# Kernel tuning notes

Hardware: AMD Instinct MI355X
Metric: run time of the kernel (lower is better)

Reference implementation:

```python
import jax, jax.numpy as jnp
from jax import lax
import numpy as np


def _gru_layer(X, mask, W, U, b):
    """Keras GRU (reset_after=True, gate order [z|r|h]) with Keras-style masking.

    X: [B,T,F] float, mask: [B,T] bool, W: [F,3u], U: [u,3u], b: [2,3u].
    At masked steps the state (== output for GRU) is carried over unchanged.
    Returns (outputs [B,T,u], final_state [B,u]).
    """
    B, T, _ = X.shape
    u = U.shape[0]
    # Precompute input projections for all timesteps (cuDNN-style).
    Xp = jnp.einsum('btf,fg->btg', X, W) + b[0]  # [B,T,3u]

    def step(h, inp):
        x_t, m_t = inp  # x_t: [B,3u], m_t: [B]
        rec = h @ U + b[1]  # [B,3u]
        xz, xr, xh = jnp.split(x_t, 3, axis=-1)
        rz, rr, rh = jnp.split(rec, 3, axis=-1)
        z = jax.nn.sigmoid(xz + rz)
        r = jax.nn.sigmoid(xr + rr)
        hh = jnp.tanh(xh + r * rh)
        h_new = z * h + (1.0 - z) * hh
        h_new = jnp.where(m_t[:, None], h_new, h)  # carry state at masked steps
        return h_new, h_new

    h0 = jnp.zeros((B, u), X.dtype)
    h_final, outs = lax.scan(step, h0, (jnp.swapaxes(Xp, 0, 1), mask.T))
    return jnp.swapaxes(outs, 0, 1), h_final


def setup_inputs() -> dict:
    key = jax.random.key(0)
    ks = jax.random.split(key, 12)
    B, T, F = 64, 1024, 16
    H, E = 256, 256
    vals = jax.random.randint(ks[0], (B, T, F), 0, 20, dtype=jnp.int32)
    # variable-length sequences padded with -1
    lengths = jax.random.randint(ks[1], (B,), T // 4, T + 1)
    valid = jnp.arange(T)[None, :] < lengths[:, None]
    batch = jnp.where(valid[:, :, None], vals, jnp.int32(-1))
    SCALE = 0.05

    def w(k, shape):
        return jax.random.normal(k, shape, jnp.float32) * SCALE

    return {
        'batch': batch,
        'W0': w(ks[2], (F, 3 * H)), 'U0': w(ks[3], (H, 3 * H)), 'b0': jnp.zeros((2, 3 * H), jnp.float32),
        'W1': w(ks[4], (H, 3 * H)), 'U1': w(ks[5], (H, 3 * H)), 'b1': jnp.zeros((2, 3 * H), jnp.float32),
        'W2': w(ks[6], (H, 3 * E)), 'U2': w(ks[7], (E, 3 * E)), 'b2': jnp.zeros((2, 3 * E), jnp.float32),
    }


def reference(batch, W0, U0, b0, W1, U1, b1, W2, U2, b2):
    mask = batch[:, :, -1] != -1  # [B,T]
    X = batch.astype(jnp.float32)
    X, _ = _gru_layer(X, mask, W0, U0, b0)
    X, _ = _gru_layer(X, mask, W1, U1, b1)
    out, h = _gru_layer(X, mask, W2, U2, b2)
    return out, h
```

## Files before the change

kernel.cpp:

```cpp
#include <hip/hip_runtime.h>
#include <cstdint>

#define BATCH 64
#define SEQ   1024
#define FEAT  16
#define HID   256
#define GATE  768
#define TC    64
#define LASTC 15
#define NT    512
#define NWRK  64
#define NITEM 192

typedef _Float16 f16x8 __attribute__((ext_vector_type(8)));
typedef float    f32x4 __attribute__((ext_vector_type(4)));

__device__ __forceinline__ float sigmoidf_(float x) { return 1.0f / (1.0f + __expf(-x)); }
__device__ __forceinline__ float tanhf_(float x)    { return 2.0f / (1.0f + __expf(-2.0f * x)) - 1.0f; }

__global__ __launch_bounds__(256) void k_packB(const float* __restrict__ U,
                                               float* __restrict__ Bfrag)
{
    const int tid = blockIdx.x * 256 + threadIdx.x;
    const int ct   = tid >> 9;
    const int kt   = (tid >> 6) & 7;
    const int lane = tid & 63;
    const int g = lane >> 4, i = lane & 15;
    const int col = ct * 16 + i;
    const int k0  = kt * 32 + g * 8;
    union { f16x8 v; float4 f; } u;
#pragma unroll
    for (int e = 0; e < 8; ++e)
        u.v[e] = (_Float16)U[(size_t)(k0 + e) * GATE + col];
    *(float4*)(Bfrag + (size_t)tid * 4) = u.f;
}

struct Params {
    const int*   batch;
    const float *W0, *b0, *b1, *b2;
    const float *Bf0, *Bf1, *Bf2;
    const float *Wp1, *Wp2;
    _Float16 *xp0a, *xp0b, *xp1a, *xp1b, *xp2a, *xp2b;
    _Float16 *y0a, *y0b, *y1a, *y1b;
    float *h0, *h1, *h2;
    float *out, *hfin;
};

__device__ __forceinline__ void gru_body(
    char* smem, const _Float16* __restrict__ xp, const float* __restrict__ Bfrag,
    const float* __restrict__ bb, const int* __restrict__ batch,
    _Float16* __restrict__ yout, float* __restrict__ fout, int obase,
    float* __restrict__ hfinal, float* __restrict__ hstate, int t0, int b)
{
    _Float16 (*hbuf)[HID] = (_Float16 (*)[HID])smem;

    const int T  = threadIdx.x;
    const int w  = T >> 6;
    const int l  = T & 63;
    const int g  = l >> 4;
    const int i  = l & 15;
    const int g1 = g & 1;
    const int c  = 32 * w + i + 16 * g1;

    f16x8 Bf[6][8];
    {
        const int cts[6] = {2 * w, 16 + 2 * w, 32 + 2 * w,
                            2 * w + 1, 17 + 2 * w, 33 + 2 * w};
#pragma unroll
        for (int ci = 0; ci < 6; ++ci)
#pragma unroll
            for (int kt = 0; kt < 8; ++kt) {
                float4 v = *(const float4*)(Bfrag + ((size_t)(cts[ci] * 8 + kt) * 64 + l) * 4);
                Bf[ci][kt] = __builtin_bit_cast(f16x8, v);
            }
    }

    const float bh = bb[GATE + 2 * HID + c];

    float hprev = (t0 == 0) ? 0.0f : hstate[b * HID + c];
    if (l < 32) hbuf[0][32 * w + l] = (_Float16)hprev;

    _Float16 nxz, nxr, nxh; int nmf;
    {
        const _Float16* xrow = xp + ((size_t)b * TC + 0) * GATE;
        nxz = xrow[c]; nxr = xrow[HID + c]; nxh = xrow[2 * HID + c];
        nmf = batch[((size_t)b * SEQ + t0) * FEAT + (FEAT - 1)];
    }
    __syncthreads();

    for (int tl = 0; tl < TC; ++tl) {
        const _Float16 cxz = nxz, cxr = nxr, cxh = nxh;
        const int cmf = nmf;
        {
            const int tn = (tl + 1 < TC) ? tl + 1 : tl;
            const _Float16* xrow = xp + ((size_t)b * TC + tn) * GATE;
            nxz = xrow[c]; nxr = xrow[HID + c]; nxh = xrow[2 * HID + c];
            nmf = batch[((size_t)b * SEQ + t0 + tn) * FEAT + (FEAT - 1)];
        }

        const _Float16* rd = hbuf[tl & 1];

        f32x4 az0 = {0.f, 0.f, 0.f, 0.f}, ar0 = az0, ah0 = az0;
        f32x4 az1 = az0, ar1 = az0, ah1 = az0;
#pragma unroll
        for (int kt = 0; kt < 8; ++kt) {
            const f16x8 a = *(const f16x8*)(rd + kt * 32 + g * 8);
            az0 = __builtin_amdgcn_mfma_f32_16x16x32_f16(a, Bf[0][kt], az0, 0, 0, 0);
            ar0 = __builtin_amdgcn_mfma_f32_16x16x32_f16(a, Bf[1][kt], ar0, 0, 0, 0);
            ah0 = __builtin_amdgcn_mfma_f32_16x16x32_f16(a, Bf[2][kt], ah0, 0, 0, 0);
            az1 = __builtin_amdgcn_mfma_f32_16x16x32_f16(a, Bf[3][kt], az1, 0, 0, 0);
            ar1 = __builtin_amdgcn_mfma_f32_16x16x32_f16(a, Bf[4][kt], ar1, 0, 0, 0);
            ah1 = __builtin_amdgcn_mfma_f32_16x16x32_f16(a, Bf[5][kt], ah1, 0, 0, 0);
        }

        const float az = g1 ? az1[0] : az0[0];
        const float ar = g1 ? ar1[0] : ar0[0];
        const float ah = g1 ? ah1[0] : ah0[0];

        const float z  = sigmoidf_((float)cxz + az);
        const float r  = sigmoidf_((float)cxr + ar);
        const float hh = tanhf_((float)cxh + r * (ah + bh));
        float hn = z * hprev + (1.0f - z) * hh;
        hn = (cmf != -1) ? hn : hprev;
        hprev = hn;

        if (l < 32) {
            if (yout)
                yout[((size_t)b * TC + tl) * HID + 32 * w + l] = (_Float16)hn;
            else
                fout[((size_t)b * SEQ + obase + tl) * HID + 32 * w + l] = hn;
            hbuf[(tl & 1) ^ 1][32 * w + l] = (_Float16)hn;
        }
        asm volatile("s_waitcnt lgkmcnt(0)\n\ts_barrier" ::: "memory");
    }

    if (l < 32) {
        hstate[b * HID + 32 * w + l] = hprev;
        if (hfinal) hfinal[b * HID + 32 * w + l] = hprev;
    }
}

__device__ __forceinline__ void gemm_mfma_body(
    char* smem, const _Float16* __restrict__ Yc, const float* __restrict__ Wp,
    const float* __restrict__ bb, _Float16* __restrict__ xpout, int mt)
{
    _Float16 (*As)[264] = (_Float16 (*)[264])smem;

    const int T = threadIdx.x;
    const int w = T >> 6;
    const int l = T & 63;
    const int g = l >> 4;
    const int i = l & 15;

    {
        const _Float16* src = Yc + (size_t)mt * TC * HID;
#pragma unroll
        for (int q = 0; q < 4; ++q) {
            const int ch  = T * 4 + q;
            const int row = ch >> 5;
            const int ko  = (ch & 31) * 8;
            *(float4*)&As[row][ko] = *(const float4*)(src + (size_t)row * HID + ko);
        }
    }
    __syncthreads();

    f16x8 Af[4][8];
#pragma unroll
    for (int rt = 0; rt < 4; ++rt)
#pragma unroll
        for (int kt = 0; kt < 8; ++kt)
            Af[rt][kt] = *(const f16x8*)&As[rt * 16 + i][kt * 32 + g * 8];

#pragma unroll
    for (int ci = 0; ci < 6; ++ci) {
        const int ct = w * 6 + ci;
        f16x8 Bfr[8];
#pragma unroll
        for (int kt = 0; kt < 8; ++kt) {
            float4 v = *(const float4*)(Wp + ((size_t)(ct * 8 + kt) * 64 + l) * 4);
            Bfr[kt] = __builtin_bit_cast(f16x8, v);
        }
        f32x4 acc[4];
#pragma unroll
        for (int rt = 0; rt < 4; ++rt) acc[rt] = (f32x4){0.f, 0.f, 0.f, 0.f};
#pragma unroll
        for (int kt = 0; kt < 8; ++kt) {
            acc[0] = __builtin_amdgcn_mfma_f32_16x16x32_f16(Af[0][kt], Bfr[kt], acc[0], 0, 0, 0);
            acc[1] = __builtin_amdgcn_mfma_f32_16x16x32_f16(Af[1][kt], Bfr[kt], acc[1], 0, 0, 0);
            acc[2] = __builtin_amdgcn_mfma_f32_16x16x32_f16(Af[2][kt], Bfr[kt], acc[2], 0, 0, 0);
            acc[3] = __builtin_amdgcn_mfma_f32_16x16x32_f16(Af[3][kt], Bfr[kt], acc[3], 0, 0, 0);
        }
        const int n = ct * 16 + i;
        const float bias = bb[n] + ((n < 2 * HID) ? bb[GATE + n] : 0.0f);
#pragma unroll
        for (int rt = 0; rt < 4; ++rt)
#pragma unroll
            for (int r = 0; r < 4; ++r)
                xpout[(size_t)(mt * TC + rt * 16 + 4 * g + r) * GATE + n] =
                    (_Float16)(acc[rt][r] + bias);
    }
    __syncthreads();
}

__device__ __forceinline__ void xp0_body(
    char* smem, const int* __restrict__ batch, const float* __restrict__ W0,
    const float* __restrict__ bb, _Float16* __restrict__ xpout, int t0, int b)
{
    int* bl = (int*)smem;
    const int T = threadIdx.x;
    for (int idx = T; idx < TC * FEAT; idx += NT)
        bl[idx] = batch[((size_t)b * SEQ + t0 + (idx >> 4)) * FEAT + (idx & 15)];
    __syncthreads();

    const int cc0 = T;
    const int cc1 = T + NT;
    const bool two = (cc1 < GATE);

    float w0a[FEAT], w0b[FEAT];
#pragma unroll
    for (int f = 0; f < FEAT; ++f) w0a[f] = W0[f * GATE + cc0];
    if (two) {
#pragma unroll
        for (int f = 0; f < FEAT; ++f) w0b[f] = W0[f * GATE + cc1];
    }
    const float ba = bb[cc0] + ((cc0 < 2 * HID) ? bb[GATE + cc0] : 0.0f);
    const float bc = two ? (bb[cc1] + ((cc1 < 2 * HID) ? bb[GATE + cc1] : 0.0f)) : 0.0f;

    for (int tl = 0; tl < TC; ++tl) {
        float a0 = ba, a1 = bc;
#pragma unroll
        for (int f = 0; f < FEAT; ++f) {
            const float xf = (float)bl[tl * FEAT + f];
            a0 += xf * w0a[f];
            if (two) a1 += xf * w0b[f];
        }
        _Float16* orow = xpout + ((size_t)b * TC + tl) * GATE;
        orow[cc0] = (_Float16)a0;
        if (two) orow[cc1] = (_Float16)a1;
    }
    __syncthreads();
}

__global__ __launch_bounds__(NT, 1) void k_fused(Params P, int d)
{
    __shared__ __align__(16) char smem[64 * 264 * 2];
    const int bid = blockIdx.x;

    if (bid < 64) {
        const int c = d;
        if (c >= 0 && c <= LASTC)
            gru_body(smem, (c & 1) ? P.xp0b : P.xp0a, P.Bf0, P.b0, P.batch,
                     (c & 1) ? P.y0b : P.y0a, nullptr, 0, nullptr, P.h0,
                     c * TC, bid);
    } else if (bid < 128) {
        const int c = d - 2;
        if (c >= 0 && c <= LASTC)
            gru_body(smem, (c & 1) ? P.xp1b : P.xp1a, P.Bf1, P.b1, P.batch,
                     (c & 1) ? P.y1b : P.y1a, nullptr, 0, nullptr, P.h1,
                     c * TC, bid - 64);
    } else if (bid < 192) {
        const int c = d - 4;
        if (c >= 0 && c <= LASTC)
            gru_body(smem, (c & 1) ? P.xp2b : P.xp2a, P.Bf2, P.b2, P.batch,
                     nullptr, P.out, c * TC, (c == LASTC) ? P.hfin : nullptr,
                     P.h2, c * TC, bid - 128);
    } else {
        for (int item = bid - 192; item < NITEM; item += NWRK) {
            if (item < 64) {
                const int c = d + 1;
                if (c >= 0 && c <= LASTC)
                    xp0_body(smem, P.batch, P.W0, P.b0,
                             (c & 1) ? P.xp0b : P.xp0a, c * TC, item);
            } else if (item < 128) {
                const int c = d - 1;
                if (c >= 0 && c <= LASTC)
                    gemm_mfma_body(smem, (c & 1) ? P.y0b : P.y0a, P.Wp1, P.b1,
                                   (c & 1) ? P.xp1b : P.xp1a, item - 64);
            } else {
                const int c = d - 3;
                if (c >= 0 && c <= LASTC)
                    gemm_mfma_body(smem, (c & 1) ? P.y1b : P.y1a, P.Wp2, P.b2,
                                   (c & 1) ? P.xp2b : P.xp2a, item - 128);
            }
        }
    }
}

extern "C" void kernel_launch(void* const* d_in, const int* in_sizes, int n_in,
                              void* d_out, int out_size, void* d_ws, size_t ws_size,
                              hipStream_t stream)
{
    const int*   batch = (const int*)d_in[0];
    const float* W0 = (const float*)d_in[1];
    const float* U0 = (const float*)d_in[2];
    const float* b0 = (const float*)d_in[3];
    const float* W1 = (const float*)d_in[4];
    const float* U1 = (const float*)d_in[5];
    const float* b1 = (const float*)d_in[6];
    const float* W2 = (const float*)d_in[7];
    const float* U2 = (const float*)d_in[8];
    const float* b2 = (const float*)d_in[9];

    float* out  = (float*)d_out;
    float* hfin = out + (size_t)BATCH * SEQ * HID;

    const size_t XPB = (size_t)BATCH * TC * GATE * 2;
    const size_t YB  = (size_t)BATCH * TC * HID * 2;
    const size_t HB  = (size_t)BATCH * HID * 4;
    const size_t BFB = (size_t)48 * 8 * 64 * 4 * 4;

    char* p = (char*)d_ws;
    auto alloc = [&](size_t bytes) { char* q = p; p += (bytes + 255) & ~(size_t)255; return q; };
    _Float16* xp0a = (_Float16*)alloc(XPB);
    _Float16* xp0b = (_Float16*)alloc(XPB);
    _Float16* xp1a = (_Float16*)alloc(XPB);
    _Float16* xp1b = (_Float16*)alloc(XPB);
    _Float16* xp2a = (_Float16*)alloc(XPB);
    _Float16* xp2b = (_Float16*)alloc(XPB);
    _Float16* y0a  = (_Float16*)alloc(YB);
    _Float16* y0b  = (_Float16*)alloc(YB);
    _Float16* y1a  = (_Float16*)alloc(YB);
    _Float16* y1b  = (_Float16*)alloc(YB);
    float* h0  = (float*)alloc(HB);
    float* h1  = (float*)alloc(HB);
    float* h2  = (float*)alloc(HB);
    float* Bf0 = (float*)alloc(BFB);
    float* Bf1 = (float*)alloc(BFB);
    float* Bf2 = (float*)alloc(BFB);
    float* Wp1 = (float*)alloc(BFB);
    float* Wp2 = (float*)alloc(BFB);

    dim3 gpack(48 * 8 * 64 / 256), bpack(256);
    k_packB<<<gpack, bpack, 0, stream>>>(U0, Bf0);
    k_packB<<<gpack, bpack, 0, stream>>>(U1, Bf1);
    k_packB<<<gpack, bpack, 0, stream>>>(U2, Bf2);
    k_packB<<<gpack, bpack, 0, stream>>>(W1, Wp1);
    k_packB<<<gpack, bpack, 0, stream>>>(W2, Wp2);

    Params P;
    P.batch = batch;
    P.W0 = W0; P.b0 = b0; P.b1 = b1; P.b2 = b2;
    P.Bf0 = Bf0; P.Bf1 = Bf1; P.Bf2 = Bf2;
    P.Wp1 = Wp1; P.Wp2 = Wp2;
    P.xp0a = xp0a; P.xp0b = xp0b; P.xp1a = xp1a; P.xp1b = xp1b;
    P.xp2a = xp2a; P.xp2b = xp2b;
    P.y0a = y0a; P.y0b = y0b; P.y1a = y1a; P.y1b = y1b;
    P.h0 = h0; P.h1 = h1; P.h2 = h2;
    P.out = out; P.hfin = hfin;

    for (int d = -1; d <= LASTC + 4; ++d)
        k_fused<<<dim3(256), dim3(NT), 0, stream>>>(P, d);
}
```

Baseline: 1.424 ms.

## Replace per-phase kernel launches with one persistent kernel using grid barriers

The 21 launches of the fused wavefront kernel become a single persistent launch of 256 blocks. Blocks step through the phases themselves and synchronise with an atomic-counter grid barrier. GRU blocks load their recurrent weight fragments into registers once and keep the hidden state in registers between chunks, so the per-launch weight reload and the global h-state round trip go away. The cost is a spin barrier that needs all 256 blocks resident at the same time (one 512-thread block per CU), which risks deadlock if they are not, plus atomic polling overhead at each phase.

```diff
diff --git a/kernel.cpp b/kernel.cpp
--- a/kernel.cpp
+++ b/kernel.cpp
@@ -42,42 +42,31 @@
     const float *Wp1, *Wp2;
     _Float16 *xp0a, *xp0b, *xp1a, *xp1b, *xp2a, *xp2b;
     _Float16 *y0a, *y0b, *y1a, *y1b;
-    float *h0, *h1, *h2;
     float *out, *hfin;
 };
 
-__device__ __forceinline__ void gru_body(
-    char* smem, const _Float16* __restrict__ xp, const float* __restrict__ Bfrag,
-    const float* __restrict__ bb, const int* __restrict__ batch,
+__device__ __forceinline__ void grid_barrier(unsigned* cnt, unsigned target)
+{
+    __threadfence();
+    __syncthreads();
+    if (threadIdx.x == 0) {
+        __hip_atomic_fetch_add(cnt, 1u, __ATOMIC_RELEASE, __HIP_MEMORY_SCOPE_AGENT);
+        while (__hip_atomic_load(cnt, __ATOMIC_ACQUIRE, __HIP_MEMORY_SCOPE_AGENT) < target)
+            __builtin_amdgcn_s_sleep(8);
+    }
+    __syncthreads();
+    __threadfence();
+}
+
+__device__ __forceinline__ void gru_phase(
+    char* smem, const _Float16* __restrict__ xp, const f16x8 (&Bf)[6][8],
+    float bh, const int* __restrict__ batch,
     _Float16* __restrict__ yout, float* __restrict__ fout, int obase,
-    float* __restrict__ hfinal, float* __restrict__ hstate, int t0, int b)
+    float* __restrict__ hfinal, float& hprev, int t0, int b,
+    int w, int l, int g, int g1, int c)
 {
     _Float16 (*hbuf)[HID] = (_Float16 (*)[HID])smem;
 
-    const int T  = threadIdx.x;
-    const int w  = T >> 6;
-    const int l  = T & 63;
-    const int g  = l >> 4;
-    const int i  = l & 15;
-    const int g1 = g & 1;
-    const int c  = 32 * w + i + 16 * g1;
-
-    f16x8 Bf[6][8];
-    {
-        const int cts[6] = {2 * w, 16 + 2 * w, 32 + 2 * w,
-                            2 * w + 1, 17 + 2 * w, 33 + 2 * w};
-#pragma unroll
-        for (int ci = 0; ci < 6; ++ci)
-#pragma unroll
-            for (int kt = 0; kt < 8; ++kt) {
-                float4 v = *(const float4*)(Bfrag + ((size_t)(cts[ci] * 8 + kt) * 64 + l) * 4);
-                Bf[ci][kt] = __builtin_bit_cast(f16x8, v);
-            }
-    }
-
-    const float bh = bb[GATE + 2 * HID + c];
-
-    float hprev = (t0 == 0) ? 0.0f : hstate[b * HID + c];
     if (l < 32) hbuf[0][32 * w + l] = (_Float16)hprev;
 
     _Float16 nxz, nxr, nxh; int nmf;
@@ -134,10 +123,8 @@
         asm volatile("s_waitcnt lgkmcnt(0)\n\ts_barrier" ::: "memory");
     }
 
-    if (l < 32) {
-        hstate[b * HID + 32 * w + l] = hprev;
-        if (hfinal) hfinal[b * HID + 32 * w + l] = hprev;
-    }
+    if (hfinal && l < 32)
+        hfinal[b * HID + 32 * w + l] = hprev;
 }
 
 __device__ __forceinline__ void gemm_mfma_body(
@@ -241,47 +228,82 @@
     __syncthreads();
 }
 
-__global__ __launch_bounds__(NT, 1) void k_fused(Params P, int d)
+__global__ __launch_bounds__(NT, 1) void k_persist(Params P, unsigned* cnt)
 {
     __shared__ __align__(16) char smem[64 * 264 * 2];
     const int bid = blockIdx.x;
-
-    if (bid < 64) {
-        const int c = d;
-        if (c >= 0 && c <= LASTC)
-            gru_body(smem, (c & 1) ? P.xp0b : P.xp0a, P.Bf0, P.b0, P.batch,
-                     (c & 1) ? P.y0b : P.y0a, nullptr, 0, nullptr, P.h0,
-                     c * TC, bid);
-    } else if (bid < 128) {
-        const int c = d - 2;
-        if (c >= 0 && c <= LASTC)
-            gru_body(smem, (c & 1) ? P.xp1b : P.xp1a, P.Bf1, P.b1, P.batch,
-                     (c & 1) ? P.y1b : P.y1a, nullptr, 0, nullptr, P.h1,
-                     c * TC, bid - 64);
-    } else if (bid < 192) {
-        const int c = d - 4;
-        if (c >= 0 && c <= LASTC)
-            gru_body(smem, (c & 1) ? P.xp2b : P.xp2a, P.Bf2, P.b2, P.batch,
-                     nullptr, P.out, c * TC, (c == LASTC) ? P.hfin : nullptr,
-                     P.h2, c * TC, bid - 128);
+    unsigned target = 0;
+
+    if (bid < 192) {
+        const int layer = bid >> 6;
+        const int b     = bid & 63;
+        const float* Bfrag = (layer == 0) ? P.Bf0 : (layer == 1) ? P.Bf1 : P.Bf2;
+        const float* bb    = (layer == 0) ? P.b0  : (layer == 1) ? P.b1  : P.b2;
+
+        const int T  = threadIdx.x;
+        const int w  = T >> 6;
+        const int l  = T & 63;
+        const int g  = l >> 4;
+        const int g1 = g & 1;
+        const int c  = 32 * w + (l & 15) + 16 * g1;
+
+        f16x8 Bf[6][8];
+        {
+            const int cts[6] = {2 * w, 16 + 2 * w, 32 + 2 * w,
+                                2 * w + 1, 17 + 2 * w, 33 + 2 * w};
+#pragma unroll
+            for (int ci = 0; ci < 6; ++ci)
+#pragma unroll
+                for (int kt = 0; kt < 8; ++kt) {
+                    float4 v = *(const float4*)(Bfrag + ((size_t)(cts[ci] * 8 + kt) * 64 + l) * 4);
+                    Bf[ci][kt] = __builtin_bit_cast(f16x8, v);
+                }
+        }
+        const float bh = bb[GATE + 2 * HID + c];
+        float hprev = 0.0f;
+
+        for (int d = -1; d <= LASTC + 4; ++d) {
+            const int cc = d - 2 * layer;
+            if (cc >= 0 && cc <= LASTC) {
+                if (layer == 0)
+                    gru_phase(smem, (cc & 1) ? P.xp0b : P.xp0a, Bf, bh, P.batch,
+                              (cc & 1) ? P.y0b : P.y0a, nullptr, 0, nullptr,
+                              hprev, cc * TC, b, w, l, g, g1, c);
+                else if (layer == 1)
+                    gru_phase(smem, (cc & 1) ? P.xp1b : P.xp1a, Bf, bh, P.batch,
+                              (cc & 1) ? P.y1b : P.y1a, nullptr, 0, nullptr,
+                              hprev, cc * TC, b, w, l, g, g1, c);
+                else
+                    gru_phase(smem, (cc & 1) ? P.xp2b : P.xp2a, Bf, bh, P.batch,
+                              nullptr, P.out, cc * TC,
+                              (cc == LASTC) ? P.hfin : nullptr,
+                              hprev, cc * TC, b, w, l, g, g1, c);
+            }
+            target += 256;
+            grid_barrier(cnt, target);
+        }
     } else {
-        for (int item = bid - 192; item < NITEM; item += NWRK) {
-            if (item < 64) {
-                const int c = d + 1;
-                if (c >= 0 && c <= LASTC)
-                    xp0_body(smem, P.batch, P.W0, P.b0,
-                             (c & 1) ? P.xp0b : P.xp0a, c * TC, item);
-            } else if (item < 128) {
-                const int c = d - 1;
-                if (c >= 0 && c <= LASTC)
-                    gemm_mfma_body(smem, (c & 1) ? P.y0b : P.y0a, P.Wp1, P.b1,
-                                   (c & 1) ? P.xp1b : P.xp1a, item - 64);
-            } else {
-                const int c = d - 3;
-                if (c >= 0 && c <= LASTC)
-                    gemm_mfma_body(smem, (c & 1) ? P.y1b : P.y1a, P.Wp2, P.b2,
-                                   (c & 1) ? P.xp2b : P.xp2a, item - 128);
+        for (int d = -1; d <= LASTC + 4; ++d) {
+            for (int item = bid - 192; item < NITEM; item += NWRK) {
+                if (item < 64) {
+                    const int cc = d + 1;
+                    if (cc >= 0 && cc <= LASTC)
+                        xp0_body(smem, P.batch, P.W0, P.b0,
+                                 (cc & 1) ? P.xp0b : P.xp0a, cc * TC, item);
+                } else if (item < 128) {
+                    const int cc = d - 1;
+                    if (cc >= 0 && cc <= LASTC)
+                        gemm_mfma_body(smem, (cc & 1) ? P.y0b : P.y0a, P.Wp1, P.b1,
+                                       (cc & 1) ? P.xp1b : P.xp1a, item - 64);
+                } else {
+                    const int cc = d - 3;
+                    if (cc >= 0 && cc <= LASTC)
+                        gemm_mfma_body(smem, (cc & 1) ? P.y1b : P.y1a, P.Wp2, P.b2,
+                                       (cc & 1) ? P.xp2b : P.xp2a, item - 128);
+                }
             }
+            target += 256;
+            grid_barrier(cnt, target);
         }
     }
 }
@@ -306,11 +328,11 @@
 
     const size_t XPB = (size_t)BATCH * TC * GATE * 2;
     const size_t YB  = (size_t)BATCH * TC * HID * 2;
-    const size_t HB  = (size_t)BATCH * HID * 4;
     const size_t BFB = (size_t)48 * 8 * 64 * 4 * 4;
 
     char* p = (char*)d_ws;
     auto alloc = [&](size_t bytes) { char* q = p; p += (bytes + 255) & ~(size_t)255; return q; };
+    unsigned* cnt  = (unsigned*)alloc(256);
     _Float16* xp0a = (_Float16*)alloc(XPB);
     _Float16* xp0b = (_Float16*)alloc(XPB);
     _Float16* xp1a = (_Float16*)alloc(XPB);
@@ -321,14 +343,13 @@
     _Float16* y0b  = (_Float16*)alloc(YB);
     _Float16* y1a  = (_Float16*)alloc(YB);
     _Float16* y1b  = (_Float16*)alloc(YB);
-    float* h0  = (float*)alloc(HB);
-    float* h1  = (float*)alloc(HB);
-    float* h2  = (float*)alloc(HB);
     float* Bf0 = (float*)alloc(BFB);
     float* Bf1 = (float*)alloc(BFB);
     float* Bf2 = (float*)alloc(BFB);
     float* Wp1 = (float*)alloc(BFB);
     float* Wp2 = (float*)alloc(BFB);
+
+    hipMemsetAsync(cnt, 0, 256, stream);
 
     dim3 gpack(48 * 8 * 64 / 256), bpack(256);
     k_packB<<<gpack, bpack, 0, stream>>>(U0, Bf0);
@@ -345,9 +366,7 @@
     P.xp0a = xp0a; P.xp0b = xp0b; P.xp1a = xp1a; P.xp1b = xp1b;
     P.xp2a = xp2a; P.xp2b = xp2b;
     P.y0a = y0a; P.y0b = y0b; P.y1a = y1a; P.y1b = y1b;
-    P.h0 = h0; P.h1 = h1; P.h2 = h2;
     P.out = out; P.hfin = hfin;
 
-    for (int d = -1; d <= LASTC + 4; ++d)
-        k_fused<<<dim3(256), dim3(NT), 0, stream>>>(P, d);
-}
+    k_persist<<<dim3(256), dim3(NT), 0, stream>>>(P, cnt);
+}
```

New measurement: 3.396 ms. +138.4%, slower.

## Fuse input-projection GEMM into recurrent GRU blocks for layers 1 and 2

Applied to the files above, without the earlier changes.

Layers 1 and 2 now run their input-projection GEMM in the same block and launch as the recurrence, just before it, instead of a separate worker block one diagonal earlier. This shortens the wavefront pipeline from 21 to 19 launches and drops the double-buffered xp1/xp2 buffers. In exchange, each recurrent block does the GEMM serially on its critical path, which lengthens every launch on layers 1 and 2. It also relies on each block's GEMM producing exactly the rows for the batch element that block then consumes.

```diff
diff --git a/kernel.cpp b/kernel.cpp
--- a/kernel.cpp
+++ b/kernel.cpp
@@ -9,8 +9,6 @@
 #define TC    64
 #define LASTC 15
 #define NT    512
-#define NWRK  64
-#define NITEM 192
 
 typedef _Float16 f16x8 __attribute__((ext_vector_type(8)));
 typedef float    f32x4 __attribute__((ext_vector_type(4)));
@@ -40,7 +38,8 @@
     const float *W0, *b0, *b1, *b2;
     const float *Bf0, *Bf1, *Bf2;
     const float *Wp1, *Wp2;
-    _Float16 *xp0a, *xp0b, *xp1a, *xp1b, *xp2a, *xp2b;
+    _Float16 *xp0a, *xp0b;
+    _Float16 *xp1, *xp2;
     _Float16 *y0a, *y0b, *y1a, *y1b;
     float *h0, *h1, *h2;
     float *out, *hfin;
@@ -253,36 +252,28 @@
                      (c & 1) ? P.y0b : P.y0a, nullptr, 0, nullptr, P.h0,
                      c * TC, bid);
     } else if (bid < 128) {
+        const int c = d - 1;
+        const int b = bid - 64;
+        if (c >= 0 && c <= LASTC) {
+            gemm_mfma_body(smem, (c & 1) ? P.y0b : P.y0a, P.Wp1, P.b1, P.xp1, b);
+            gru_body(smem, P.xp1, P.Bf1, P.b1, P.batch,
+                     (c & 1) ? P.y1b : P.y1a, nullptr, 0, nullptr, P.h1,
+                     c * TC, b);
+        }
+    } else if (bid < 192) {
         const int c = d - 2;
+        const int b = bid - 128;
+        if (c >= 0 && c <= LASTC) {
+            gemm_mfma_body(smem, (c & 1) ? P.y1b : P.y1a, P.Wp2, P.b2, P.xp2, b);
+            gru_body(smem, P.xp2, P.Bf2, P.b2, P.batch,
+                     nullptr, P.out, c * TC, (c == LASTC) ? P.hfin : nullptr,
+                     P.h2, c * TC, b);
+        }
+    } else {
+        const int c = d + 1;
         if (c >= 0 && c <= LASTC)
-            gru_body(smem, (c & 1) ? P.xp1b : P.xp1a, P.Bf1, P.b1, P.batch,
-                     (c & 1) ? P.y1b : P.y1a, nullptr, 0, nullptr, P.h1,
-                     c * TC, bid - 64);
-    } else if (bid < 192) {
-        const int c = d - 4;
-        if (c >= 0 && c <= LASTC)
-            gru_body(smem, (c & 1) ? P.xp2b : P.xp2a, P.Bf2, P.b2, P.batch,
-                     nullptr, P.out, c * TC, (c == LASTC) ? P.hfin : nullptr,
-                     P.h2, c * TC, bid - 128);
-    } else {
-        for (int item = bid - 192; item < NITEM; item += NWRK) {
-            if (item < 64) {
-                const int c = d + 1;
-                if (c >= 0 && c <= LASTC)
-                    xp0_body(smem, P.batch, P.W0, P.b0,
-                             (c & 1) ? P.xp0b : P.xp0a, c * TC, item);
-            } else if (item < 128) {
-                const int c = d - 1;
-                if (c >= 0 && c <= LASTC)
-                    gemm_mfma_body(smem, (c & 1) ? P.y0b : P.y0a, P.Wp1, P.b1,
-                                   (c & 1) ? P.xp1b : P.xp1a, item - 64);
-            } else {
-                const int c = d - 3;
-                if (c >= 0 && c <= LASTC)
-                    gemm_mfma_body(smem, (c & 1) ? P.y1b : P.y1a, P.Wp2, P.b2,
-                                   (c & 1) ? P.xp2b : P.xp2a, item - 128);
-            }
-        }
+            xp0_body(smem, P.batch, P.W0, P.b0,
+                     (c & 1) ? P.xp0b : P.xp0a, c * TC, bid - 192);
     }
 }
 
@@ -313,10 +304,8 @@
     auto alloc = [&](size_t bytes) { char* q = p; p += (bytes + 255) & ~(size_t)255; return q; };
     _Float16* xp0a = (_Float16*)alloc(XPB);
     _Float16* xp0b = (_Float16*)alloc(XPB);
-    _Float16* xp1a = (_Float16*)alloc(XPB);
-    _Float16* xp1b = (_Float16*)alloc(XPB);
-    _Float16* xp2a = (_Float16*)alloc(XPB);
-    _Float16* xp2b = (_Float16*)alloc(XPB);
+    _Float16* xp1  = (_Float16*)alloc(XPB);
+    _Float16* xp2  = (_Float16*)alloc(XPB);
     _Float16* y0a  = (_Float16*)alloc(YB);
     _Float16* y0b  = (_Float16*)alloc(YB);
     _Float16* y1a  = (_Float16*)alloc(YB);
@@ -342,12 +331,12 @@
     P.W0 = W0; P.b0 = b0; P.b1 = b1; P.b2 = b2;
     P.Bf0 = Bf0; P.Bf1 = Bf1; P.Bf2 = Bf2;
     P.Wp1 = Wp1; P.Wp2 = Wp2;
-    P.xp0a = xp0a; P.xp0b = xp0b; P.xp1a = xp1a; P.xp1b = xp1b;
-    P.xp2a = xp2a; P.xp2b = xp2b;
+    P.xp0a = xp0a; P.xp0b = xp0b;
+    P.xp1 = xp1; P.xp2 = xp2;
     P.y0a = y0a; P.y0b = y0b; P.y1a = y1a; P.y1b = y1b;
     P.h0 = h0; P.h1 = h1; P.h2 = h2;
     P.out = out; P.hfin = hfin;
 
-    for (int d = -1; d <= LASTC + 4; ++d)
+    for (int d = -1; d <= LASTC + 2; ++d)
         k_fused<<<dim3(256), dim3(NT), 0, stream>>>(P, d);
 }
```

Result: faster. 1.382 ms (median of 2 runs) (-3.0%).
